# Optimization experiments

Measured on AMD Instinct MI355X. Metric: run time of the kernel, lower is better.

## Reference

```python
import jax, jax.numpy as jnp
import numpy as np

N = 50000          # num nodes
E = 800000         # num edges
IN_C = 256
HID = 128
OUT_C = 2
R = 8              # num_relations
B = 4              # num_bases
L = 3              # n_layers
ALPHA = 0.1


def setup_inputs() -> dict:
    key = jax.random.key(0)
    ks = jax.random.split(key, 12)
    x = jax.random.normal(ks[0], (N, IN_C), dtype=jnp.float32)
    edge_index = jax.random.randint(ks[1], (2, E), 0, N, dtype=jnp.int64)
    edge_type = jax.random.randint(ks[2], (E,), 0, R, dtype=jnp.int64)
    # parameters
    lin1_w = jax.random.normal(ks[3], (IN_C, HID), dtype=jnp.float32) * (1.0 / np.sqrt(IN_C))
    lin1_b = jnp.zeros((HID,), dtype=jnp.float32)
    bases = jax.random.normal(ks[4], (L, B, HID, HID), dtype=jnp.float32) * (1.0 / np.sqrt(HID))
    comp = jax.random.normal(ks[5], (L, R, B), dtype=jnp.float32) * (1.0 / np.sqrt(B))
    root = jax.random.normal(ks[6], (L, HID, HID), dtype=jnp.float32) * (1.0 / np.sqrt(HID))
    bias_conv = jnp.zeros((L, HID), dtype=jnp.float32)
    lin2_w = jax.random.normal(ks[7], (HID, OUT_C), dtype=jnp.float32) * (1.0 / np.sqrt(HID))
    lin2_b = jnp.zeros((OUT_C,), dtype=jnp.float32)
    # GPR-style temp init: temp[k] = alpha*(1-alpha)^k, temp[K] = (1-alpha)^K
    temp = ALPHA * (1.0 - ALPHA) ** np.arange(L + 1)
    temp[-1] = (1.0 - ALPHA) ** L
    temp = jnp.asarray(temp, dtype=jnp.float32)
    return {"x": x, "edge_index": edge_index, "edge_type": edge_type,
            "lin1_w": lin1_w, "lin1_b": lin1_b, "bases": bases, "comp": comp,
            "root": root, "bias_conv": bias_conv, "lin2_w": lin2_w,
            "lin2_b": lin2_b, "temp": temp}


def rgcn_conv(x, bases_l, comp_l, root_l, bias_l, src, dst, edge_type):
    # basis decomposition: W_r = sum_b comp[r,b] * bases[b]   -> [R, HID, HID]
    W = jnp.einsum('rb,bio->rio', comp_l, bases_l)
    out = x @ root_l + bias_l                      # root/self transform + bias
    for r in range(R):                             # fixed small relation set
        mask = (edge_type == r)
        h = x @ W[r]                               # [N, HID] relation transform
        msg = jnp.where(mask[:, None], h[src], 0.0)  # [E, HID] gathered messages
        agg = jax.ops.segment_sum(msg, dst, num_segments=N)
        cnt = jax.ops.segment_sum(mask.astype(x.dtype), dst, num_segments=N)
        out = out + agg / jnp.maximum(cnt, 1.0)[:, None]   # mean aggregation
    return out


def reference(x, edge_index, edge_type, lin1_w, lin1_b, bases, comp, root,
              bias_conv, lin2_w, lin2_b, temp):
    src, dst = edge_index[0], edge_index[1]
    h = jax.nn.relu(x @ lin1_w + lin1_b)           # pre_transform=False path; dropout=identity (eval)
    hidden = h * temp[0]
    cur = hidden
    for i in range(L):
        cur = rgcn_conv(cur, bases[i], comp[i], root[i], bias_conv[i], src, dst, edge_type)
        if i < L - 1:
            cur = jax.nn.relu(cur)
        hidden = hidden + temp[i + 1] * cur
    return hidden @ lin2_w + lin2_b                # [N, OUT_C]
```

## Files before the change

### kernel.cpp

```cpp
#include <hip/hip_runtime.h>

#define Nn   50000
#define Ee   800000
#define INC  256
#define HIDd 128
#define RR   8
#define BB   4
#define LL   3
#define RN   (RR * Nn)
#define NCH  391

typedef _Float16 f16;
typedef _Float16 f16x2 __attribute__((ext_vector_type(2)));
typedef _Float16 f16x4 __attribute__((ext_vector_type(4)));
typedef _Float16 f16x8 __attribute__((ext_vector_type(8)));
typedef float    f32x4 __attribute__((ext_vector_type(4)));

static inline size_t align256(size_t x) { return (x + 255) & ~(size_t)255; }


__global__ void count_k(const int* __restrict__ ei, const int* __restrict__ et,
                        int* __restrict__ cnt) {
    int e = blockIdx.x * 256 + threadIdx.x;
    if (e < Ee) {
        int d = ei[Ee + e];
        int r = et[e];
        atomicAdd(&cnt[r * Nn + d], 1);
    }
}

__global__ __launch_bounds__(256) void chunksum_k(const int* __restrict__ cnt,
                                                  int* __restrict__ csum) {
    int c = blockIdx.x;
    int t = threadIdx.x;
    int idx4 = c * 256 + t;
    int s = 0;
    if (idx4 < RN / 4) {
        int4 v = ((const int4*)cnt)[idx4];
        s = v.x + v.y + v.z + v.w;
    }
#pragma unroll
    for (int o = 1; o < 64; o <<= 1) s += __shfl_xor(s, o);
    __shared__ int ws[4];
    if ((t & 63) == 0) ws[t >> 6] = s;
    __syncthreads();
    if (t == 0) csum[c] = ws[0] + ws[1] + ws[2] + ws[3];
}

__global__ __launch_bounds__(512) void chunkscan_k(const int* __restrict__ csum,
                                                   int* __restrict__ cbase,
                                                   int* __restrict__ off) {
    __shared__ int lds[NCH];
    int t = threadIdx.x;
    if (t < NCH) lds[t] = csum[t];
    __syncthreads();
    if (t == 0) {
        int run = 0;
        for (int i = 0; i < NCH; ++i) { int v = lds[i]; lds[i] = run; run += v; }
        off[RN] = run;
    }
    __syncthreads();
    if (t < NCH) cbase[t] = lds[t];
}

__global__ __launch_bounds__(256) void writeoff_k(const int* __restrict__ cnt,
                                                  const int* __restrict__ cbase,
                                                  int* __restrict__ off,
                                                  int* __restrict__ cursor,
                                                  float* __restrict__ invc) {
    int c = blockIdx.x;
    int t = threadIdx.x;
    int idx4 = c * 256 + t;
    bool ok = idx4 < RN / 4;
    int4 v = make_int4(0, 0, 0, 0);
    if (ok) v = ((const int4*)cnt)[idx4];
    int s = v.x + v.y + v.z + v.w;
    int lane = t & 63;
    int incl = s;
#pragma unroll
    for (int o = 1; o < 64; o <<= 1) {
        int u = __shfl_up(incl, o);
        if (lane >= o) incl += u;
    }
    __shared__ int wsum[4];
    if (lane == 63) wsum[t >> 6] = incl;
    __syncthreads();
    int w = t >> 6;
    int wpre = 0;
    if (w > 0) wpre += wsum[0];
    if (w > 1) wpre += wsum[1];
    if (w > 2) wpre += wsum[2];
    int excl = cbase[c] + wpre + incl - s;
    if (ok) {
        int o0 = excl;
        int o1 = o0 + v.x;
        int o2 = o1 + v.y;
        int o3 = o2 + v.z;
        int4 ov = make_int4(o0, o1, o2, o3);
        ((int4*)off)[idx4] = ov;
        ((int4*)cursor)[idx4] = ov;
        float4 iv;
        iv.x = 1.0f / (float)(v.x > 1 ? v.x : 1);
        iv.y = 1.0f / (float)(v.y > 1 ? v.y : 1);
        iv.z = 1.0f / (float)(v.z > 1 ? v.z : 1);
        iv.w = 1.0f / (float)(v.w > 1 ? v.w : 1);
        ((float4*)invc)[idx4] = iv;
    }
}

__global__ void scatter_k(const int* __restrict__ ei, const int* __restrict__ et,
                          int* __restrict__ cursor, int* __restrict__ es) {
    int e = blockIdx.x * 256 + threadIdx.x;
    if (e < Ee) {
        int s = ei[e];
        int d = ei[Ee + e];
        int r = et[e];
        int p = atomicAdd(&cursor[r * Nn + d], 1);
        es[p] = s;
    }
}


__global__ void makewT_k(const float* __restrict__ bases, const float* __restrict__ root,
                         f16* __restrict__ WT) {
    int idx = blockIdx.x * 256 + threadIdx.x;
    int l = idx / (5 * 16384);
    int rem = idx % (5 * 16384);
    int c = rem >> 14;
    int n = (rem >> 7) & 127;
    int k = rem & 127;
    float v = (c == 0) ? root[l * 16384 + k * 128 + n]
                       : bases[((l * BB + (c - 1)) << 14) + k * 128 + n];
    WT[idx] = (f16)v;
}


__global__ void castx_k(const float* __restrict__ x, f16* __restrict__ xh) {
    int i = blockIdx.x * 256 + threadIdx.x;
    float4 v = ((const float4*)x)[i];
    f16x4 o;
    o[0] = (f16)v.x; o[1] = (f16)v.y; o[2] = (f16)v.z; o[3] = (f16)v.w;
    *(f16x4*)(xh + (size_t)i * 4) = o;
}


__global__ void makew1T_k(const float* __restrict__ w1, f16* __restrict__ w1hT) {
    int idx = blockIdx.x * 256 + threadIdx.x;
    int n = idx >> 8, k = idx & 255;
    w1hT[idx] = (f16)w1[k * 128 + n];
}


__global__ __launch_bounds__(256, 2) void lin1m_k(const f16* __restrict__ xh,
                                                  const f16* __restrict__ w1hT,
                                                  const float* __restrict__ b1,
                                                  const float* __restrict__ temp,
                                                  float* __restrict__ hidden,
                                                  f16* __restrict__ curh) {
    __shared__ f16 Ah[128 * 136];
    __shared__ f16 Bh[128 * 136];
    int t = threadIdx.x;
    int v0 = blockIdx.x * 128;
    int w = t >> 6, lane = t & 63;
    int wr = w >> 1, wc = w & 1;
    int l15 = lane & 15, l4 = lane >> 4;
    int srow = t >> 1, sseg = t & 1;

    f32x4 acc[4][4] = {};

    for (int c = 0; c < 2; ++c) {
        __syncthreads();
        {
            f16* dst = Ah + srow * 136 + sseg * 64;
            if (v0 + srow < Nn) {
                const f16* src = xh + (size_t)(v0 + srow) * INC + c * 128 + sseg * 64;
#pragma unroll
                for (int j = 0; j < 8; ++j)
                    *(f16x8*)(dst + j * 8) = *(const f16x8*)(src + j * 8);
            } else {
                f16x8 z = {};
#pragma unroll
                for (int j = 0; j < 8; ++j)
                    *(f16x8*)(dst + j * 8) = z;
            }
        }
        {
            const f16* src = w1hT + srow * 256 + c * 128 + sseg * 64;
            f16* dst = Bh + srow * 136 + sseg * 64;
#pragma unroll
            for (int j = 0; j < 8; ++j)
                *(f16x8*)(dst + j * 8) = *(const f16x8*)(src + j * 8);
        }
        __syncthreads();
#pragma unroll
        for (int ks = 0; ks < 4; ++ks) {
            f16x8 af[4], bf[4];
#pragma unroll
            for (int mf = 0; mf < 4; ++mf)
                af[mf] = *(const f16x8*)(Ah + (wr * 64 + mf * 16 + l15) * 136 + ks * 32 + l4 * 8);
#pragma unroll
            for (int nf = 0; nf < 4; ++nf)
                bf[nf] = *(const f16x8*)(Bh + (wc * 64 + nf * 16 + l15) * 136 + ks * 32 + l4 * 8);
#pragma unroll
            for (int mf = 0; mf < 4; ++mf)
#pragma unroll
                for (int nf = 0; nf < 4; ++nf)
                    acc[mf][nf] = __builtin_amdgcn_mfma_f32_16x16x32_f16(af[mf], bf[nf], acc[mf][nf], 0, 0, 0);
        }
    }

    __syncthreads();
    float t0 = temp[0];
    float bs[4];
#pragma unroll
    for (int nf = 0; nf < 4; ++nf) bs[nf] = b1[wc * 64 + nf * 16 + l15];
#pragma unroll
    for (int mf = 0; mf < 4; ++mf)
#pragma unroll
        for (int nf = 0; nf < 4; ++nf)
#pragma unroll
            for (int j = 0; j < 4; ++j) {
                float val = fmaxf(acc[mf][nf][j] + bs[nf], 0.f) * t0;
                Ah[(wr * 64 + mf * 16 + l4 * 4 + j) * 136 + wc * 64 + nf * 16 + l15] = (f16)val;
            }
    __syncthreads();
    if (v0 + srow < Nn) {
        size_t gb = (size_t)(v0 + srow) * HIDd + sseg * 64;
        const f16* cr = Ah + srow * 136 + sseg * 64;
#pragma unroll
        for (int j = 0; j < 8; ++j)
            *(f16x8*)(curh + gb + j * 8) = *(const f16x8*)(cr + j * 8);
        float* hp = hidden + gb;
#pragma unroll
        for (int j = 0; j < 16; ++j) {
            float4 h;
            h.x = (float)cr[j * 4 + 0];
            h.y = (float)cr[j * 4 + 1];
            h.z = (float)cr[j * 4 + 2];
            h.w = (float)cr[j * 4 + 3];
            *(float4*)(hp + j * 4) = h;
        }
    }
}


__global__ __launch_bounds__(256) void meanr_k(const f16* __restrict__ curh,
                                               const int* __restrict__ es,
                                               const int* __restrict__ off,
                                               const float* __restrict__ invc,
                                               const float* __restrict__ comp_l,
                                               f16* __restrict__ aggb) {
    __shared__ float ms[2][8][128];
    int t = threadIdx.x;
    int sub = t >> 7;
    int r = (t >> 4) & 7;
    int lane = t & 15;
    int d = blockIdx.x * 2 + sub;
    int g = r * Nn + d;
    int e0 = off[g], e1 = off[g + 1];
    float iv = invc[g];
    float acc[8] = {};
    const f16* cb = curh + lane * 8;
    int e = e0;
    for (; e + 4 <= e1; e += 4) {
        int s0 = es[e], s1 = es[e + 1], s2 = es[e + 2], s3 = es[e + 3];
        f16x8 v0 = *(const f16x8*)(cb + (size_t)s0 * HIDd);
        f16x8 v1 = *(const f16x8*)(cb + (size_t)s1 * HIDd);
        f16x8 v2 = *(const f16x8*)(cb + (size_t)s2 * HIDd);
        f16x8 v3 = *(const f16x8*)(cb + (size_t)s3 * HIDd);
#pragma unroll
        for (int j = 0; j < 8; ++j)
            acc[j] += (float)v0[j] + (float)v1[j] + (float)v2[j] + (float)v3[j];
    }
    for (; e < e1; ++e) {
        int s = es[e];
        f16x8 v = *(const f16x8*)(cb + (size_t)s * HIDd);
#pragma unroll
        for (int j = 0; j < 8; ++j) acc[j] += (float)v[j];
    }
    float4 p0, p1;
    p0.x = acc[0] * iv; p0.y = acc[1] * iv; p0.z = acc[2] * iv; p0.w = acc[3] * iv;
    p1.x = acc[4] * iv; p1.y = acc[5] * iv; p1.z = acc[6] * iv; p1.w = acc[7] * iv;
    *(float4*)&ms[sub][r][lane * 8]     = p0;
    *(float4*)&ms[sub][r][lane * 8 + 4] = p1;
    __syncthreads();
    int k = t & 127;
    float m[8];
#pragma unroll
    for (int rr = 0; rr < 8; ++rr) m[rr] = ms[sub][rr][k];
    f16* op = aggb + ((size_t)d * 4) * HIDd + k;
#pragma unroll
    for (int b = 0; b < 4; ++b) {
        float o = 0.f;
#pragma unroll
        for (int rr = 0; rr < 8; ++rr) o += comp_l[rr * 4 + b] * m[rr];
        op[b * HIDd] = (f16)o;
    }
}


__global__ __launch_bounds__(256, 2) void gemm_k(const f16* __restrict__ curh,
                                                 const f16* __restrict__ aggb,
                                                 const f16* __restrict__ WTl,
                                                 const float* __restrict__ bias,
                                                 const float* __restrict__ temp, int tidx,
                                                 f16* __restrict__ curh_next,
                                                 float* __restrict__ hidden,
                                                 int dorelu) {
    __shared__ f16 Ah[128 * 136];
    __shared__ f16 Bh[128 * 136];
    int t = threadIdx.x;
    int v0 = blockIdx.x * 128;
    int w = t >> 6, lane = t & 63;
    int wr = w >> 1, wc = w & 1;
    int l15 = lane & 15, l4 = lane >> 4;
    int srow = t >> 1, sseg = t & 1;

    f32x4 acc[4][4] = {};

    for (int c = 0; c < 5; ++c) {
        __syncthreads();
        {
            f16* dst = Ah + srow * 136 + sseg * 64;
            if (v0 + srow < Nn) {
                const f16* src = (c == 0)
                    ? curh + (size_t)(v0 + srow) * HIDd + sseg * 64
                    : aggb + ((size_t)(v0 + srow) * 4 + (c - 1)) * HIDd + sseg * 64;
#pragma unroll
                for (int j = 0; j < 8; ++j)
                    *(f16x8*)(dst + j * 8) = *(const f16x8*)(src + j * 8);
            } else {
                f16x8 z = {};
#pragma unroll
                for (int j = 0; j < 8; ++j)
                    *(f16x8*)(dst + j * 8) = z;
            }
        }
        {
            const f16* src = WTl + (c << 14) + srow * HIDd + sseg * 64;
            f16* dst = Bh + srow * 136 + sseg * 64;
#pragma unroll
            for (int j = 0; j < 8; ++j)
                *(f16x8*)(dst + j * 8) = *(const f16x8*)(src + j * 8);
        }
        __syncthreads();
#pragma unroll
        for (int ks = 0; ks < 4; ++ks) {
            f16x8 af[4], bf[4];
#pragma unroll
            for (int mf = 0; mf < 4; ++mf)
                af[mf] = *(const f16x8*)(Ah + (wr * 64 + mf * 16 + l15) * 136 + ks * 32 + l4 * 8);
#pragma unroll
            for (int nf = 0; nf < 4; ++nf)
                bf[nf] = *(const f16x8*)(Bh + (wc * 64 + nf * 16 + l15) * 136 + ks * 32 + l4 * 8);
#pragma unroll
            for (int mf = 0; mf < 4; ++mf)
#pragma unroll
                for (int nf = 0; nf < 4; ++nf)
                    acc[mf][nf] = __builtin_amdgcn_mfma_f32_16x16x32_f16(af[mf], bf[nf], acc[mf][nf], 0, 0, 0);
        }
    }

    __syncthreads();
    float tl = temp[tidx];
    float bs[4];
#pragma unroll
    for (int nf = 0; nf < 4; ++nf) bs[nf] = bias[wc * 64 + nf * 16 + l15];
#pragma unroll
    for (int mf = 0; mf < 4; ++mf)
#pragma unroll
        for (int nf = 0; nf < 4; ++nf)
#pragma unroll
            for (int j = 0; j < 4; ++j) {
                float val = acc[mf][nf][j] + bs[nf];
                if (dorelu) val = fmaxf(val, 0.f);
                Ah[(wr * 64 + mf * 16 + l4 * 4 + j) * 136 + wc * 64 + nf * 16 + l15] = (f16)val;
            }
    __syncthreads();
    if (v0 + srow < Nn) {
        size_t gb = (size_t)(v0 + srow) * HIDd + sseg * 64;
        const f16* cr = Ah + srow * 136 + sseg * 64;
#pragma unroll
        for (int j = 0; j < 8; ++j)
            *(f16x8*)(curh_next + gb + j * 8) = *(const f16x8*)(cr + j * 8);
        float* hp = hidden + gb;
#pragma unroll
        for (int j = 0; j < 16; ++j) {
            float4 h = *(float4*)(hp + j * 4);
            h.x += tl * (float)cr[j * 4 + 0];
            h.y += tl * (float)cr[j * 4 + 1];
            h.z += tl * (float)cr[j * 4 + 2];
            h.w += tl * (float)cr[j * 4 + 3];
            *(float4*)(hp + j * 4) = h;
        }
    }
}


__global__ __launch_bounds__(256) void lin2_k(const float* __restrict__ hidden,
                                              const float* __restrict__ w2,
                                              const float* __restrict__ b2,
                                              float* __restrict__ out) {
    __shared__ float ws[256];
    __shared__ float bs[2];
    int t = threadIdx.x;
    ws[t] = w2[t & 255];
    if (t < 2) bs[t] = b2[t];
    __syncthreads();
    int node = blockIdx.x * 64 + (t >> 2);
    int q = t & 3;
    float a0 = 0.f, a1 = 0.f;
    if (node < Nn) {
        const float* hp = hidden + (size_t)node * HIDd + q * 32;
#pragma unroll
        for (int kk = 0; kk < 32; kk += 4) {
            float4 h = *(const float4*)(hp + kk);
            int kb = (q * 32 + kk) * 2;
            a0 += h.x * ws[kb]     + h.y * ws[kb + 2] + h.z * ws[kb + 4] + h.w * ws[kb + 6];
            a1 += h.x * ws[kb + 1] + h.y * ws[kb + 3] + h.z * ws[kb + 5] + h.w * ws[kb + 7];
        }
    }
    a0 += __shfl_xor(a0, 1); a0 += __shfl_xor(a0, 2);
    a1 += __shfl_xor(a1, 1); a1 += __shfl_xor(a1, 2);
    if (node < Nn && q == 0) {
        out[node * 2 + 0] = a0 + bs[0];
        out[node * 2 + 1] = a1 + bs[1];
    }
}


extern "C" void kernel_launch(void* const* d_in, const int* in_sizes, int n_in,
                              void* d_out, int out_size, void* d_ws, size_t ws_size,
                              hipStream_t stream) {
    (void)in_sizes; (void)n_in; (void)out_size; (void)ws_size;
    const float* x        = (const float*)d_in[0];
    const int*   ei       = (const int*)d_in[1];
    const int*   et       = (const int*)d_in[2];
    const float* lin1_w   = (const float*)d_in[3];
    const float* lin1_b   = (const float*)d_in[4];
    const float* bases    = (const float*)d_in[5];
    const float* comp     = (const float*)d_in[6];
    const float* root     = (const float*)d_in[7];
    const float* bias_cv  = (const float*)d_in[8];
    const float* lin2_w   = (const float*)d_in[9];
    const float* lin2_b   = (const float*)d_in[10];
    const float* temp     = (const float*)d_in[11];
    float* out = (float*)d_out;

    char* w = (char*)d_ws;
    int*   off    = (int*)w;    w += align256((size_t)(RN + 1) * 4);
    int*   cnt    = (int*)w;    w += align256((size_t)RN * 4);
    int*   cursor = (int*)w;    w += align256((size_t)RN * 4);
    float* invc   = (float*)w;  w += align256((size_t)RN * 4);
    int*   csum   = (int*)w;    w += align256((size_t)NCH * 4);
    int*   cbase  = (int*)w;    w += align256((size_t)NCH * 4);
    int*   es     = (int*)w;    w += align256((size_t)Ee * 4);
    f16*   WT     = (f16*)w;    w += align256((size_t)LL * 5 * HIDd * HIDd * 2);
    f16*   w1hT   = (f16*)w;    w += align256((size_t)HIDd * INC * 2);
    f16*   xh     = (f16*)w;    w += align256((size_t)Nn * INC * 2);
    float* hidden = (float*)w;  w += align256((size_t)Nn * HIDd * 4);
    f16*   curh   = (f16*)w;    w += align256((size_t)Nn * HIDd * 2);
    f16*   aggb   = (f16*)w;    w += align256((size_t)Nn * 4 * HIDd * 2);

    hipMemsetAsync(cnt, 0, (size_t)RN * 4, stream);
    count_k<<<(Ee + 255) / 256, 256, 0, stream>>>(ei, et, cnt);
    chunksum_k<<<NCH, 256, 0, stream>>>(cnt, csum);
    chunkscan_k<<<1, 512, 0, stream>>>(csum, cbase, off);
    writeoff_k<<<NCH, 256, 0, stream>>>(cnt, cbase, off, cursor, invc);
    scatter_k<<<(Ee + 255) / 256, 256, 0, stream>>>(ei, et, cursor, es);
    makewT_k<<<(LL * 5 * 16384) / 256, 256, 0, stream>>>(bases, root, WT);
    castx_k<<<(Nn * INC / 4) / 256, 256, 0, stream>>>(x, xh);
    makew1T_k<<<(HIDd * INC) / 256, 256, 0, stream>>>(lin1_w, w1hT);
    lin1m_k<<<(Nn + 127) / 128, 256, 0, stream>>>(xh, w1hT, lin1_b, temp, hidden, curh);

    for (int l = 0; l < LL; ++l) {
        meanr_k<<<Nn / 2, 256, 0, stream>>>(curh, es, off, invc, comp + l * RR * BB, aggb);
        gemm_k<<<(Nn + 127) / 128, 256, 0, stream>>>(
            curh, aggb, WT + (size_t)l * 5 * 16384, bias_cv + l * HIDd,
            temp, l + 1, curh, hidden, (l < LL - 1) ? 1 : 0);
    }
    lin2_k<<<(Nn + 63) / 64, 256, 0, stream>>>(hidden, lin2_w, lin2_b, out);
}
```

Measured before the change: 508.7 us.

## Fold lin2 projection into per-layer epilogues and fuse fp16 cast into lin1

Because lin2 is linear, hidden@W2 equals the sum of temp-weighted per-layer projections, so each GEMM epilogue now projects its output tile to two values and accumulates them into out. This removes the fp32 hidden buffer entirely, along with its 25 MB read-modify-write per layer and the separate lin2 kernel. The fp32-to-fp16 cast of x is also moved into lin1's tile load, which drops the castx kernel and its intermediate buffer. The cost is extra per-row dot-product work in each epilogue, and the projection now runs on fp16-rounded activations.

After: 459.6 us. 1.11x faster.

```diff
diff --git a/kernel.cpp b/kernel.cpp
--- a/kernel.cpp
+++ b/kernel.cpp
@@ -135,15 +135,6 @@
 }
 
 
-__global__ void castx_k(const float* __restrict__ x, f16* __restrict__ xh) {
-    int i = blockIdx.x * 256 + threadIdx.x;
-    float4 v = ((const float4*)x)[i];
-    f16x4 o;
-    o[0] = (f16)v.x; o[1] = (f16)v.y; o[2] = (f16)v.z; o[3] = (f16)v.w;
-    *(f16x4*)(xh + (size_t)i * 4) = o;
-}
-
-
 __global__ void makew1T_k(const float* __restrict__ w1, f16* __restrict__ w1hT) {
     int idx = blockIdx.x * 256 + threadIdx.x;
     int n = idx >> 8, k = idx & 255;
@@ -151,14 +142,18 @@
 }
 
 
-__global__ __launch_bounds__(256, 2) void lin1m_k(const f16* __restrict__ xh,
+__global__ __launch_bounds__(256, 2) void lin1m_k(const float* __restrict__ x,
                                                   const f16* __restrict__ w1hT,
                                                   const float* __restrict__ b1,
                                                   const float* __restrict__ temp,
-                                                  float* __restrict__ hidden,
-                                                  f16* __restrict__ curh) {
+                                                  const float* __restrict__ w2,
+                                                  const float* __restrict__ b2,
+                                                  f16* __restrict__ curh,
+                                                  float* __restrict__ out) {
     __shared__ f16 Ah[128 * 136];
     __shared__ f16 Bh[128 * 136];
+    __shared__ float ws2[256];
+    __shared__ float bsh[2];
     int t = threadIdx.x;
     int v0 = blockIdx.x * 128;
     int w = t >> 6, lane = t & 63;
@@ -166,6 +161,9 @@
     int l15 = lane & 15, l4 = lane >> 4;
     int srow = t >> 1, sseg = t & 1;
 
+    ws2[t] = w2[t];
+    if (t < 2) bsh[t] = b2[t];
+
     f32x4 acc[4][4] = {};
 
     for (int c = 0; c < 2; ++c) {
@@ -173,10 +171,14 @@
         {
             f16* dst = Ah + srow * 136 + sseg * 64;
             if (v0 + srow < Nn) {
-                const f16* src = xh + (size_t)(v0 + srow) * INC + c * 128 + sseg * 64;
-#pragma unroll
-                for (int j = 0; j < 8; ++j)
-                    *(f16x8*)(dst + j * 8) = *(const f16x8*)(src + j * 8);
+                const float* src = x + (size_t)(v0 + srow) * INC + c * 128 + sseg * 64;
+#pragma unroll
+                for (int j = 0; j < 16; ++j) {
+                    float4 f = *(const float4*)(src + j * 4);
+                    f16x4 o;
+                    o[0] = (f16)f.x; o[1] = (f16)f.y; o[2] = (f16)f.z; o[3] = (f16)f.w;
+                    *(f16x4*)(dst + j * 4) = o;
+                }
             } else {
                 f16x8 z = {};
 #pragma unroll
@@ -230,16 +232,28 @@
 #pragma unroll
         for (int j = 0; j < 8; ++j)
             *(f16x8*)(curh + gb + j * 8) = *(const f16x8*)(cr + j * 8);
-        float* hp = hidden + gb;
-#pragma unroll
-        for (int j = 0; j < 16; ++j) {
-            float4 h;
-            h.x = (float)cr[j * 4 + 0];
-            h.y = (float)cr[j * 4 + 1];
-            h.z = (float)cr[j * 4 + 2];
-            h.w = (float)cr[j * 4 + 3];
-            *(float4*)(hp + j * 4) = h;
-        }
+        float d0 = 0.f, d1 = 0.f;
+#pragma unroll
+        for (int q = 0; q < 8; ++q) {
+            f16x8 cv = *(const f16x8*)(cr + q * 8);
+            const float* wp = &ws2[sseg * 128 + q * 16];
+#pragma unroll
+            for (int j = 0; j < 8; ++j) {
+                float c = (float)cv[j];
+                d0 += c * wp[j * 2];
+                d1 += c * wp[j * 2 + 1];
+            }
+        }
+        d0 += __shfl_xor(d0, 1);
+        d1 += __shfl_xor(d1, 1);
+        if (sseg == 0) {
+            out[(v0 + srow) * 2 + 0] = bsh[0] + d0;
+            out[(v0 + srow) * 2 + 1] = bsh[1] + d1;
+        }
+    } else {
+        float d0 = 0.f, d1 = 0.f;
+        d0 += __shfl_xor(d0, 1);
+        d1 += __shfl_xor(d1, 1);
     }
 }
 
@@ -304,17 +318,21 @@
                                                  const f16* __restrict__ WTl,
                                                  const float* __restrict__ bias,
                                                  const float* __restrict__ temp, int tidx,
+                                                 const float* __restrict__ w2,
                                                  f16* __restrict__ curh_next,
-                                                 float* __restrict__ hidden,
+                                                 float* __restrict__ out,
                                                  int dorelu) {
     __shared__ f16 Ah[128 * 136];
     __shared__ f16 Bh[128 * 136];
+    __shared__ float ws2[256];
     int t = threadIdx.x;
     int v0 = blockIdx.x * 128;
     int w = t >> 6, lane = t & 63;
     int wr = w >> 1, wc = w & 1;
     int l15 = lane & 15, l4 = lane >> 4;
     int srow = t >> 1, sseg = t & 1;
+
+    ws2[t] = w2[t];
 
     f32x4 acc[4][4] = {};
 
@@ -383,48 +401,28 @@
 #pragma unroll
         for (int j = 0; j < 8; ++j)
             *(f16x8*)(curh_next + gb + j * 8) = *(const f16x8*)(cr + j * 8);
-        float* hp = hidden + gb;
-#pragma unroll
-        for (int j = 0; j < 16; ++j) {
-            float4 h = *(float4*)(hp + j * 4);
-            h.x += tl * (float)cr[j * 4 + 0];
-            h.y += tl * (float)cr[j * 4 + 1];
-            h.z += tl * (float)cr[j * 4 + 2];
-            h.w += tl * (float)cr[j * 4 + 3];
-            *(float4*)(hp + j * 4) = h;
-        }
-    }
-}
-
-
-__global__ __launch_bounds__(256) void lin2_k(const float* __restrict__ hidden,
-                                              const float* __restrict__ w2,
-                                              const float* __restrict__ b2,
-                                              float* __restrict__ out) {
-    __shared__ float ws[256];
-    __shared__ float bs[2];
-    int t = threadIdx.x;
-    ws[t] = w2[t & 255];
-    if (t < 2) bs[t] = b2[t];
-    __syncthreads();
-    int node = blockIdx.x * 64 + (t >> 2);
-    int q = t & 3;
-    float a0 = 0.f, a1 = 0.f;
-    if (node < Nn) {
-        const float* hp = hidden + (size_t)node * HIDd + q * 32;
-#pragma unroll
-        for (int kk = 0; kk < 32; kk += 4) {
-            float4 h = *(const float4*)(hp + kk);
-            int kb = (q * 32 + kk) * 2;
-            a0 += h.x * ws[kb]     + h.y * ws[kb + 2] + h.z * ws[kb + 4] + h.w * ws[kb + 6];
-            a1 += h.x * ws[kb + 1] + h.y * ws[kb + 3] + h.z * ws[kb + 5] + h.w * ws[kb + 7];
-        }
-    }
-    a0 += __shfl_xor(a0, 1); a0 += __shfl_xor(a0, 2);
-    a1 += __shfl_xor(a1, 1); a1 += __shfl_xor(a1, 2);
-    if (node < Nn && q == 0) {
-        out[node * 2 + 0] = a0 + bs[0];
-        out[node * 2 + 1] = a1 + bs[1];
+        float d0 = 0.f, d1 = 0.f;
+#pragma unroll
+        for (int q = 0; q < 8; ++q) {
+            f16x8 cv = *(const f16x8*)(cr + q * 8);
+            const float* wp = &ws2[sseg * 128 + q * 16];
+#pragma unroll
+            for (int j = 0; j < 8; ++j) {
+                float c = (float)cv[j];
+                d0 += c * wp[j * 2];
+                d1 += c * wp[j * 2 + 1];
+            }
+        }
+        d0 += __shfl_xor(d0, 1);
+        d1 += __shfl_xor(d1, 1);
+        if (sseg == 0) {
+            out[(v0 + srow) * 2 + 0] += tl * d0;
+            out[(v0 + srow) * 2 + 1] += tl * d1;
+        }
+    } else {
+        float d0 = 0.f, d1 = 0.f;
+        d0 += __shfl_xor(d0, 1);
+        d1 += __shfl_xor(d1, 1);
     }
 }
 
@@ -457,8 +455,6 @@
     int*   es     = (int*)w;    w += align256((size_t)Ee * 4);
     f16*   WT     = (f16*)w;    w += align256((size_t)LL * 5 * HIDd * HIDd * 2);
     f16*   w1hT   = (f16*)w;    w += align256((size_t)HIDd * INC * 2);
-    f16*   xh     = (f16*)w;    w += align256((size_t)Nn * INC * 2);
-    float* hidden = (float*)w;  w += align256((size_t)Nn * HIDd * 4);
     f16*   curh   = (f16*)w;    w += align256((size_t)Nn * HIDd * 2);
     f16*   aggb   = (f16*)w;    w += align256((size_t)Nn * 4 * HIDd * 2);
 
@@ -469,15 +465,14 @@
     writeoff_k<<<NCH, 256, 0, stream>>>(cnt, cbase, off, cursor, invc);
     scatter_k<<<(Ee + 255) / 256, 256, 0, stream>>>(ei, et, cursor, es);
     makewT_k<<<(LL * 5 * 16384) / 256, 256, 0, stream>>>(bases, root, WT);
-    castx_k<<<(Nn * INC / 4) / 256, 256, 0, stream>>>(x, xh);
     makew1T_k<<<(HIDd * INC) / 256, 256, 0, stream>>>(lin1_w, w1hT);
-    lin1m_k<<<(Nn + 127) / 128, 256, 0, stream>>>(xh, w1hT, lin1_b, temp, hidden, curh);
+    lin1m_k<<<(Nn + 127) / 128, 256, 0, stream>>>(x, w1hT, lin1_b, temp, lin2_w, lin2_b,
+                                                  curh, out);
 
     for (int l = 0; l < LL; ++l) {
         meanr_k<<<Nn / 2, 256, 0, stream>>>(curh, es, off, invc, comp + l * RR * BB, aggb);
         gemm_k<<<(Nn + 127) / 128, 256, 0, stream>>>(
             curh, aggb, WT + (size_t)l * 5 * 16384, bias_cv + l * HIDd,
-            temp, l + 1, curh, hidden, (l < LL - 1) ? 1 : 0);
-    }
-    lin2_k<<<(Nn + 63) / 64, 256, 0, stream>>>(hidden, lin2_w, lin2_b, out);
-}
+            temp, l + 1, lin2_w, curh, out, (l < LL - 1) ? 1 : 0);
+    }
+}
```
